# Kernel tuning notes

Hardware: AMD Instinct MI355X
Metric: run time of the kernel (lower is better)

Reference implementation:

```python
import jax, jax.numpy as jnp
import numpy as np

N_NODES = 50000
N_EDGES = 800000
DROP_P = 0.1


def setup_inputs() -> dict:
    key = jax.random.key(0)
    ks = jax.random.split(key, 8)
    x = jax.random.normal(ks[0], (N_NODES, 128), dtype=jnp.float32)
    edge_index = jax.random.randint(ks[1], (2, N_EDGES), 0, N_NODES, dtype=jnp.int64)
    # SAGEConv params: lin_l (applied to aggregated neighbors, has bias), lin_r (root, no bias)
    Wl1 = jax.random.normal(ks[2], (128, 256), dtype=jnp.float32) * 0.05
    Wr1 = jax.random.normal(ks[3], (128, 256), dtype=jnp.float32) * 0.05
    b1 = jax.random.normal(ks[4], (256,), dtype=jnp.float32) * 0.05
    Wl2 = jax.random.normal(ks[5], (256, 128), dtype=jnp.float32) * 0.05
    Wr2 = jax.random.normal(ks[6], (256, 128), dtype=jnp.float32) * 0.05
    b2 = jax.random.normal(ks[7], (128,), dtype=jnp.float32) * 0.05
    return {"x": x, "edge_index": edge_index, "Wl1": Wl1, "Wr1": Wr1, "b1": b1,
            "Wl2": Wl2, "Wr2": Wr2, "b2": b2}


def _sage_conv(x, src, dst, Wl, Wr, b, n_nodes):
    # PyG SAGEConv (mean aggr): out = lin_l(mean_{j in N(i)} x_j) + lin_r(x_i)
    msg = x[src]                                                  # [E, d] gather
    agg = jax.ops.segment_sum(msg, dst, num_segments=n_nodes)    # [N, d]
    cnt = jax.ops.segment_sum(jnp.ones((src.shape[0],), x.dtype), dst, num_segments=n_nodes)
    mean = agg / jnp.maximum(cnt, 1.0)[:, None]
    return mean @ Wl + x @ Wr + b


def reference(x, edge_index, Wl1, Wr1, b1, Wl2, Wr2, b2):
    src, dst = edge_index[0], edge_index[1]
    n = x.shape[0]
    h = _sage_conv(x, src, dst, Wl1, Wr1, b1, n)
    h = jax.nn.relu(h)
    # dropout p=0.1 with deterministic key (training=True in source)
    keep = jax.random.bernoulli(jax.random.key(42), 1.0 - DROP_P, h.shape)
    h = jnp.where(keep, h / (1.0 - DROP_P), 0.0)
    return _sage_conv(h, src, dst, Wl2, Wr2, b2, n)
```

## Files before the change

kernel.cpp:

```cpp
#include <hip/hip_runtime.h>

#define NN 50000
#define NE 800000
#define NBC 49
#define MSB 391

typedef __attribute__((ext_vector_type(8))) short short8;
typedef __attribute__((ext_vector_type(4))) float f32x4;

#define GLDS(g, l)                                                              \
  __builtin_amdgcn_global_load_lds(                                             \
      (const __attribute__((address_space(1))) void*)(g),                       \
      (__attribute__((address_space(3))) void*)(l), 16, 0, 0)

__device__ __forceinline__ unsigned short f2bf(float f) {
  union { float f; unsigned u; } v; v.f = f;
  unsigned r = (v.u + 0x7FFFu + ((v.u >> 16) & 1u)) >> 16;
  return (unsigned short)r;
}
__device__ __forceinline__ float bflo(unsigned u) {
  union { unsigned x; float f; } v; v.x = u << 16; return v.f;
}
__device__ __forceinline__ float bfhi(unsigned u) {
  union { unsigned x; float f; } v; v.x = u & 0xFFFF0000u; return v.f;
}

__device__ __forceinline__ unsigned tf_rotl(unsigned x, int r) {
#if __has_builtin(__builtin_amdgcn_alignbit)
  return __builtin_amdgcn_alignbit(x, x, 32 - r);
#else
  return (x << r) | (x >> (32 - r));
#endif
}
__device__ __forceinline__ void threefry_0_42(unsigned x0, unsigned x1,
                                              unsigned& o0, unsigned& o1) {
  const unsigned k0 = 0u, k1 = 42u;
  const unsigned k2 = k0 ^ k1 ^ 0x1BD11BDAu;
  x0 += k0; x1 += k1;
#define TF_R(r) { x0 += x1; x1 = tf_rotl(x1, (r)); x1 ^= x0; }
  TF_R(13) TF_R(15) TF_R(26) TF_R(6)
  x0 += k1; x1 += k2 + 1u;
  TF_R(17) TF_R(29) TF_R(16) TF_R(24)
  x0 += k2; x1 += k0 + 2u;
  TF_R(13) TF_R(15) TF_R(26) TF_R(6)
  x0 += k0; x1 += k1 + 3u;
  TF_R(17) TF_R(29) TF_R(16) TF_R(24)
  x0 += k1; x1 += k2 + 4u;
  TF_R(13) TF_R(15) TF_R(26) TF_R(6)
  x0 += k2; x1 += k0 + 5u;
#undef TF_R
  o0 = x0; o1 = x1;
}
__device__ __forceinline__ float dropout_scale(unsigned flat) {
  unsigned o0, o1;
  threefry_0_42(0u, flat, o0, o1);
  unsigned bits = o0 ^ o1;
  return ((bits >> 9) < 7549747u) ? (1.0f / 0.9f) : 0.0f;
}

#define CVTB 6250
__global__ void prep_k(const float4* __restrict__ x, uint2* __restrict__ xb,
                       const float* __restrict__ Wl1, const float* __restrict__ Wr1,
                       const float* __restrict__ Wl2, const float* __restrict__ Wr2,
                       unsigned short* __restrict__ W1t, unsigned short* __restrict__ W2t,
                       unsigned* __restrict__ hist) {
  int bid = blockIdx.x;
  if (bid < CVTB) {
    int i = bid * 256 + threadIdx.x;
    float4 v = x[i];
    uint2 o;
    o.x = (unsigned)f2bf(v.x) | ((unsigned)f2bf(v.y) << 16);
    o.y = (unsigned)f2bf(v.z) | ((unsigned)f2bf(v.w) << 16);
    xb[i] = o;
  } else if (bid < CVTB + 512) {
    int gid = (bid - CVTB) * 256 + threadIdx.x;
    int idx = gid & 65535;
    int n = idx >> 8, k = idx & 255;
    if (gid < 65536) {
      float v = (k < 128) ? Wr1[(size_t)k * 256 + n] : Wl1[(size_t)(k - 128) * 256 + n];
      W1t[idx] = f2bf(v);
    } else {
      float v = (n < 128) ? Wl2[(size_t)k * 128 + n] : Wr2[(size_t)k * 128 + (n - 128)];
      W2t[idx] = f2bf(v);
    }
  } else {
    if (threadIdx.x < 64) hist[threadIdx.x] = 0;
  }
}

__global__ __launch_bounds__(256) void histC_k(const int* __restrict__ dst,
                                               unsigned* __restrict__ hist) {
  __shared__ unsigned lh[64];
  int tid = threadIdx.x;
  if (tid < 64) lh[tid] = 0;
  __syncthreads();
  int base = blockIdx.x * 2048;
#pragma unroll
  for (int k = 0; k < 8; ++k) {
    int e = base + k * 256 + tid;
    if (e < NE) atomicAdd(&lh[((unsigned)dst[e]) >> 10], 1u);
  }
  __syncthreads();
  if (tid < 64 && lh[tid]) atomicAdd(&hist[tid], lh[tid]);
}

__global__ __launch_bounds__(64) void scan64_k(const unsigned* __restrict__ hist,
                                               unsigned* __restrict__ bases,
                                               unsigned* __restrict__ gcur) {
  int tid = threadIdx.x;
  unsigned v = hist[tid], incl = v;
#pragma unroll
  for (int o = 1; o < 64; o <<= 1) {
    unsigned t = __shfl_up(incl, o);
    if (tid >= o) incl += t;
  }
  unsigned ex = incl - v;
  bases[tid] = ex;
  gcur[tid] = ex;
  if (tid == 63) bases[64] = incl;
}

__global__ __launch_bounds__(256) void msplit_k(const int* __restrict__ src,
                                                const int* __restrict__ dst,
                                                unsigned* __restrict__ gcur,
                                                unsigned* __restrict__ bufA) {
  __shared__ unsigned lh[64], gb[64], lc[64];
  int tid = threadIdx.x;
  if (tid < 64) { lh[tid] = 0; lc[tid] = 0; }
  __syncthreads();
  int base = blockIdx.x * 2048;
  unsigned s[8], d[8];
  bool val[8];
#pragma unroll
  for (int k = 0; k < 8; ++k) {
    int e = base + k * 256 + tid;
    val[k] = (e < NE);
    s[k] = val[k] ? (unsigned)src[e] : 0u;
    d[k] = val[k] ? (unsigned)dst[e] : 0u;
    if (val[k]) atomicAdd(&lh[d[k] >> 10], 1u);
  }
  __syncthreads();
  if (tid < 64 && lh[tid]) gb[tid] = atomicAdd(&gcur[tid], lh[tid]);
  __syncthreads();
#pragma unroll
  for (int k = 0; k < 8; ++k) {
    if (val[k]) {
      unsigned b = d[k] >> 10;
      unsigned pos = atomicAdd(&lc[b], 1u);
      bufA[gb[b] + pos] = (s[k] & 0xFFFFu) | ((d[k] & 1023u) << 16);
    }
  }
}

__global__ __launch_bounds__(1024) void passB2_k(const unsigned* __restrict__ bases,
                                                 const unsigned* __restrict__ bufA,
                                                 unsigned short* __restrict__ esrc,
                                                 unsigned* __restrict__ rowptr,
                                                 float* __restrict__ inv) {
  __shared__ unsigned cnt[1024], offs[1024], s_[1024];
  __shared__ unsigned short stage[18432];
  const int b = blockIdx.x, tid = threadIdx.x;
  const unsigned base0 = bases[b];
  const unsigned end0 = bases[b + 1];
  const unsigned bcnt = end0 - base0;

  cnt[tid] = 0;
  __syncthreads();
  for (unsigned i = tid; i < bcnt; i += 1024)
    atomicAdd(&cnt[bufA[base0 + i] >> 16], 1u);
  __syncthreads();

  unsigned c = cnt[tid];
  s_[tid] = c;
  __syncthreads();
  for (int o = 1; o < 1024; o <<= 1) {
    unsigned t = (tid >= o) ? s_[tid - o] : 0u;
    __syncthreads();
    s_[tid] += t;
    __syncthreads();
  }
  unsigned ex = s_[tid] - c;
  offs[tid] = ex;
  int node = b * 1024 + tid;
  if (node < NN) {
    rowptr[node] = base0 + ex;
    inv[node] = 1.0f / fmaxf((float)c, 1.0f);
  }
  cnt[tid] = 0;
  if (b == NBC - 1 && tid == 0) rowptr[NN] = NE;
  __syncthreads();

  if (bcnt <= 18432) {
    for (unsigned i = tid; i < bcnt; i += 1024) {
      unsigned w = bufA[base0 + i];
      unsigned dl = w >> 16;
      unsigned pos = atomicAdd(&cnt[dl], 1u);
      stage[offs[dl] + pos] = (unsigned short)w;
    }
    __syncthreads();
    for (unsigned i = tid; i < bcnt; i += 1024) esrc[base0 + i] = stage[i];
  } else {
    for (unsigned i = tid; i < bcnt; i += 1024) {
      unsigned w = bufA[base0 + i];
      unsigned dl = w >> 16;
      unsigned pos = atomicAdd(&cnt[dl], 1u);
      esrc[base0 + offs[dl] + pos] = (unsigned short)w;
    }
  }
}

__global__ __launch_bounds__(256) void gather_mean_k(
    const unsigned short* __restrict__ esrc, const unsigned* __restrict__ rowptr,
    const float* __restrict__ inv, const unsigned* __restrict__ xb,
    unsigned* __restrict__ meanb) {
  int node = blockIdx.x * 4 + (threadIdx.x >> 6);
  if (node >= NN) return;
  int lane = threadIdx.x & 63;
  unsigned beg = rowptr[node], end = rowptr[node + 1];
  float ax = 0.f, ay = 0.f;
  unsigned t = beg;
  for (; t + 8 <= end; t += 8) {
    unsigned v0 = xb[(size_t)esrc[t + 0] * 64 + lane];
    unsigned v1 = xb[(size_t)esrc[t + 1] * 64 + lane];
    unsigned v2 = xb[(size_t)esrc[t + 2] * 64 + lane];
    unsigned v3 = xb[(size_t)esrc[t + 3] * 64 + lane];
    unsigned v4 = xb[(size_t)esrc[t + 4] * 64 + lane];
    unsigned v5 = xb[(size_t)esrc[t + 5] * 64 + lane];
    unsigned v6 = xb[(size_t)esrc[t + 6] * 64 + lane];
    unsigned v7 = xb[(size_t)esrc[t + 7] * 64 + lane];
    ax += ((bflo(v0) + bflo(v1)) + (bflo(v2) + bflo(v3))) +
          ((bflo(v4) + bflo(v5)) + (bflo(v6) + bflo(v7)));
    ay += ((bfhi(v0) + bfhi(v1)) + (bfhi(v2) + bfhi(v3))) +
          ((bfhi(v4) + bfhi(v5)) + (bfhi(v6) + bfhi(v7)));
  }
  for (; t + 4 <= end; t += 4) {
    unsigned v0 = xb[(size_t)esrc[t + 0] * 64 + lane];
    unsigned v1 = xb[(size_t)esrc[t + 1] * 64 + lane];
    unsigned v2 = xb[(size_t)esrc[t + 2] * 64 + lane];
    unsigned v3 = xb[(size_t)esrc[t + 3] * 64 + lane];
    ax += (bflo(v0) + bflo(v1)) + (bflo(v2) + bflo(v3));
    ay += (bfhi(v0) + bfhi(v1)) + (bfhi(v2) + bfhi(v3));
  }
  for (; t < end; ++t) {
    unsigned v0 = xb[(size_t)esrc[t] * 64 + lane];
    ax += bflo(v0); ay += bfhi(v0);
  }
  float sc = inv[node];
  meanb[(size_t)node * 64 + lane] =
      (unsigned)f2bf(ax * sc) | ((unsigned)f2bf(ay * sc) << 16);
}

__global__ __launch_bounds__(256) void gather_add_k(
    const unsigned short* __restrict__ esrc, const unsigned* __restrict__ rowptr,
    const float* __restrict__ inv, const unsigned* __restrict__ P,
    float* __restrict__ out) {
  int node = blockIdx.x * 4 + (threadIdx.x >> 6);
  if (node >= NN) return;
  int lane = threadIdx.x & 63;
  unsigned beg = rowptr[node], end = rowptr[node + 1];
  float ax = 0.f, ay = 0.f;
  unsigned t = beg;
  for (; t + 8 <= end; t += 8) {
    unsigned v0 = P[(size_t)esrc[t + 0] * 64 + lane];
    unsigned v1 = P[(size_t)esrc[t + 1] * 64 + lane];
    unsigned v2 = P[(size_t)esrc[t + 2] * 64 + lane];
    unsigned v3 = P[(size_t)esrc[t + 3] * 64 + lane];
    unsigned v4 = P[(size_t)esrc[t + 4] * 64 + lane];
    unsigned v5 = P[(size_t)esrc[t + 5] * 64 + lane];
    unsigned v6 = P[(size_t)esrc[t + 6] * 64 + lane];
    unsigned v7 = P[(size_t)esrc[t + 7] * 64 + lane];
    ax += ((bflo(v0) + bflo(v1)) + (bflo(v2) + bflo(v3))) +
          ((bflo(v4) + bflo(v5)) + (bflo(v6) + bflo(v7)));
    ay += ((bfhi(v0) + bfhi(v1)) + (bfhi(v2) + bfhi(v3))) +
          ((bfhi(v4) + bfhi(v5)) + (bfhi(v6) + bfhi(v7)));
  }
  for (; t + 4 <= end; t += 4) {
    unsigned v0 = P[(size_t)esrc[t + 0] * 64 + lane];
    unsigned v1 = P[(size_t)esrc[t + 1] * 64 + lane];
    unsigned v2 = P[(size_t)esrc[t + 2] * 64 + lane];
    unsigned v3 = P[(size_t)esrc[t + 3] * 64 + lane];
    ax += (bflo(v0) + bflo(v1)) + (bflo(v2) + bflo(v3));
    ay += (bfhi(v0) + bfhi(v1)) + (bfhi(v2) + bfhi(v3));
  }
  for (; t < end; ++t) {
    unsigned v0 = P[(size_t)esrc[t] * 64 + lane];
    ax += bflo(v0); ay += bfhi(v0);
  }
  float sc = inv[node];
  float2* O = (float2*)out;
  float2 o = O[(size_t)node * 64 + lane];
  o.x += ax * sc;
  o.y += ay * sc;
  O[(size_t)node * 64 + lane] = o;
}


__global__ __launch_bounds__(256) void mgemm1_k(
    const unsigned short* __restrict__ xb, const unsigned short* __restrict__ meanb,
    const unsigned short* __restrict__ W1t, const float* __restrict__ b1,
    unsigned short* __restrict__ h) {
  __shared__ __align__(16) char As[64 * 64 * 2];
  __shared__ __align__(16) char Bs[64 * 64 * 2];
  const int tid = threadIdx.x;
  const int lane = tid & 63, wid = tid >> 6;
  const int wm = (wid >> 1) * 32, wn = (wid & 1) * 32;
  const int r16 = lane & 15, g = lane >> 4;
  const unsigned bid = blockIdx.x;
  const unsigned v_ = (bid & 7u) * 391u + (bid >> 3);
  const int m0 = (int)(v_ >> 2) * 64;
  const int j0 = (int)(v_ & 3u) * 64;
  const int wbase = (tid & ~63);

  const unsigned short* aSrcX[2];
  const unsigned short* aSrcM[2];
  const unsigned short* bSrc[2];
  char* ldsA[2];
  char* ldsB[2];
#pragma unroll
  for (int p = 0; p < 2; ++p) {
    int id = p * 256 + tid;
    int r = id >> 3, cb = id & 7;
    int grow = m0 + r;
    if (grow >= NN) grow = NN - 1;
    int swz = (cb ^ (r & 7)) << 3;
    aSrcX[p] = xb + (size_t)grow * 128 + swz;
    aSrcM[p] = meanb + (size_t)grow * 128 + swz;
    bSrc[p] = W1t + (size_t)(j0 + r) * 256 + swz;
    ldsA[p] = As + ((p * 256 + wbase) << 4);
    ldsB[p] = Bs + ((p * 256 + wbase) << 4);
  }

  int aoff[2][2], boff[2][2];
#pragma unroll
  for (int f = 0; f < 2; ++f)
#pragma unroll
    for (int ks = 0; ks < 2; ++ks) {
      int ar = wm + f * 16 + r16;
      aoff[f][ks] = ar * 128 + ((ks * 64 + g * 16) ^ ((ar & 7) << 4));
      int br = wn + f * 16 + r16;
      boff[f][ks] = br * 128 + ((ks * 64 + g * 16) ^ ((br & 7) << 4));
    }

  f32x4 acc[2][2] = {};

  auto compute = [&]() {
#pragma unroll
    for (int ks = 0; ks < 2; ++ks) {
      short8 af[2], bf[2];
#pragma unroll
      for (int f = 0; f < 2; ++f) {
        af[f] = *(const short8*)(As + aoff[f][ks]);
        bf[f] = *(const short8*)(Bs + boff[f][ks]);
      }
#pragma unroll
      for (int i = 0; i < 2; ++i)
#pragma unroll
        for (int j = 0; j < 2; ++j)
          acc[i][j] = __builtin_amdgcn_mfma_f32_16x16x32_bf16(af[i], bf[j], acc[i][j], 0, 0, 0);
    }
  };

  GLDS(aSrcX[0], ldsA[0]); GLDS(aSrcX[1], ldsA[1]);
  GLDS(bSrc[0], ldsB[0]);  GLDS(bSrc[1], ldsB[1]);

  float dsc[2][2][4];
#pragma unroll
  for (int i = 0; i < 2; ++i)
#pragma unroll
    for (int j = 0; j < 2; ++j) {
      int col = j0 + wn + j * 16 + r16;
#pragma unroll
      for (int q = 0; q < 4; ++q) {
        int row = m0 + wm + i * 16 + g * 4 + q;
        dsc[i][j][q] = dropout_scale((unsigned)row * 256u + (unsigned)col);
      }
    }

  __syncthreads();
  compute();
  __syncthreads();
  GLDS(aSrcX[0] + 64, ldsA[0]); GLDS(aSrcX[1] + 64, ldsA[1]);
  GLDS(bSrc[0] + 64, ldsB[0]);  GLDS(bSrc[1] + 64, ldsB[1]);
  __syncthreads();
  compute();
  __syncthreads();
  GLDS(aSrcM[0], ldsA[0]);       GLDS(aSrcM[1], ldsA[1]);
  GLDS(bSrc[0] + 128, ldsB[0]);  GLDS(bSrc[1] + 128, ldsB[1]);
  __syncthreads();
  compute();
  __syncthreads();
  GLDS(aSrcM[0] + 64, ldsA[0]);  GLDS(aSrcM[1] + 64, ldsA[1]);
  GLDS(bSrc[0] + 192, ldsB[0]);  GLDS(bSrc[1] + 192, ldsB[1]);
  __syncthreads();
  compute();

#pragma unroll
  for (int i = 0; i < 2; ++i)
#pragma unroll
    for (int j = 0; j < 2; ++j) {
      int col = j0 + wn + j * 16 + r16;
      float bias = b1[col];
#pragma unroll
      for (int q = 0; q < 4; ++q) {
        int row = m0 + wm + i * 16 + g * 4 + q;
        if (row < NN) {
          float v = fmaxf(acc[i][j][q] + bias, 0.f) * dsc[i][j][q];
          h[(size_t)row * 256 + col] = f2bf(v);
        }
      }
    }
}

__global__ __launch_bounds__(256) void mgemm2_k(
    const unsigned short* __restrict__ h, const unsigned short* __restrict__ W2t,
    const float* __restrict__ b2, unsigned short* __restrict__ P,
    float* __restrict__ out) {
  __shared__ __align__(16) char As[64 * 64 * 2];
  __shared__ __align__(16) char Bs[64 * 64 * 2];
  const int tid = threadIdx.x;
  const int lane = tid & 63, wid = tid >> 6;
  const int wm = (wid >> 1) * 32, wn = (wid & 1) * 32;
  const int r16 = lane & 15, g = lane >> 4;
  const unsigned bid = blockIdx.x;
  const unsigned v_ = (bid & 7u) * 391u + (bid >> 3);
  const int m0 = (int)(v_ >> 2) * 64;
  const int j0 = (int)(v_ & 3u) * 64;
  const int wbase = (tid & ~63);

  const unsigned short* aSrc[2];
  const unsigned short* bSrc[2];
  char* ldsA[2];
  char* ldsB[2];
#pragma unroll
  for (int p = 0; p < 2; ++p) {
    int id = p * 256 + tid;
    int r = id >> 3, cb = id & 7;
    int grow = m0 + r;
    if (grow >= NN) grow = NN - 1;
    int swz = (cb ^ (r & 7)) << 3;
    aSrc[p] = h + (size_t)grow * 256 + swz;
    bSrc[p] = W2t + (size_t)(j0 + r) * 256 + swz;
    ldsA[p] = As + ((p * 256 + wbase) << 4);
    ldsB[p] = Bs + ((p * 256 + wbase) << 4);
  }

  int aoff[2][2], boff[2][2];
#pragma unroll
  for (int f = 0; f < 2; ++f)
#pragma unroll
    for (int ks = 0; ks < 2; ++ks) {
      int ar = wm + f * 16 + r16;
      aoff[f][ks] = ar * 128 + ((ks * 64 + g * 16) ^ ((ar & 7) << 4));
      int br = wn + f * 16 + r16;
      boff[f][ks] = br * 128 + ((ks * 64 + g * 16) ^ ((br & 7) << 4));
    }

  f32x4 acc[2][2] = {};

  auto compute = [&]() {
#pragma unroll
    for (int ks = 0; ks < 2; ++ks) {
      short8 af[2], bf[2];
#pragma unroll
      for (int f = 0; f < 2; ++f) {
        af[f] = *(const short8*)(As + aoff[f][ks]);
        bf[f] = *(const short8*)(Bs + boff[f][ks]);
      }
#pragma unroll
      for (int i = 0; i < 2; ++i)
#pragma unroll
        for (int j = 0; j < 2; ++j)
          acc[i][j] = __builtin_amdgcn_mfma_f32_16x16x32_bf16(af[i], bf[j], acc[i][j], 0, 0, 0);
    }
  };

  GLDS(aSrc[0], ldsA[0]); GLDS(aSrc[1], ldsA[1]);
  GLDS(bSrc[0], ldsB[0]); GLDS(bSrc[1], ldsB[1]);
  __syncthreads();
  compute();
  __syncthreads();
  GLDS(aSrc[0] + 64, ldsA[0]); GLDS(aSrc[1] + 64, ldsA[1]);
  GLDS(bSrc[0] + 64, ldsB[0]); GLDS(bSrc[1] + 64, ldsB[1]);
  __syncthreads();
  compute();
  __syncthreads();
  GLDS(aSrc[0] + 128, ldsA[0]); GLDS(aSrc[1] + 128, ldsA[1]);
  GLDS(bSrc[0] + 128, ldsB[0]); GLDS(bSrc[1] + 128, ldsB[1]);
  __syncthreads();
  compute();
  __syncthreads();
  GLDS(aSrc[0] + 192, ldsA[0]); GLDS(aSrc[1] + 192, ldsA[1]);
  GLDS(bSrc[0] + 192, ldsB[0]); GLDS(bSrc[1] + 192, ldsB[1]);
  __syncthreads();
  compute();

#pragma unroll
  for (int i = 0; i < 2; ++i)
#pragma unroll
    for (int j = 0; j < 2; ++j) {
      int col = j0 + wn + j * 16 + r16;
#pragma unroll
      for (int q = 0; q < 4; ++q) {
        int row = m0 + wm + i * 16 + g * 4 + q;
        if (row < NN) {
          if (col < 128) {
            P[(size_t)row * 128 + col] = f2bf(acc[i][j][q]);
          } else {
            out[(size_t)row * 128 + (col - 128)] = acc[i][j][q] + b2[col - 128];
          }
        }
      }
    }
}

extern "C" void kernel_launch(void* const* d_in, const int* in_sizes, int n_in,
                              void* d_out, int out_size, void* d_ws, size_t ws_size,
                              hipStream_t stream) {
  const float* x   = (const float*)d_in[0];
  const int*   ei  = (const int*)d_in[1];
  const float* Wl1 = (const float*)d_in[2];
  const float* Wr1 = (const float*)d_in[3];
  const float* b1  = (const float*)d_in[4];
  const float* Wl2 = (const float*)d_in[5];
  const float* Wr2 = (const float*)d_in[6];
  const float* b2  = (const float*)d_in[7];
  float* out = (float*)d_out;

  const int* src = ei;
  const int* dst = ei + NE;

  char* ws = (char*)d_ws;
  unsigned*       rowptr = (unsigned*)ws;
  float*          inv    = (float*)(ws + 0x40000);
  unsigned*       hist   = (unsigned*)(ws + 0x80000);
  unsigned*       bases  = (unsigned*)(ws + 0x80400);
  unsigned*       gcur   = (unsigned*)(ws + 0x80800);
  unsigned short* esrc   = (unsigned short*)(ws + 0xC0000);
  unsigned*       bufA   = (unsigned*)(ws + 0x280000);
  unsigned short* W1t    = (unsigned short*)(ws + 0x600000);
  unsigned short* W2t    = (unsigned short*)(ws + 0x620000);
  unsigned short* xb     = (unsigned short*)(ws + 0x700000);
  unsigned short* meanb  = (unsigned short*)(ws + 0x1400000);
  unsigned short* h      = (unsigned short*)(ws + 0x2100000);
  unsigned short* P      = (unsigned short*)(ws + 0x3A00000);

  const int TPB = 256;

  prep_k<<<CVTB + 513, TPB, 0, stream>>>((const float4*)x, (uint2*)xb,
                                         Wl1, Wr1, Wl2, Wr2, W1t, W2t, hist);

  histC_k<<<MSB, TPB, 0, stream>>>(dst, hist);
  scan64_k<<<1, 64, 0, stream>>>(hist, bases, gcur);
  msplit_k<<<MSB, TPB, 0, stream>>>(src, dst, gcur, bufA);
  passB2_k<<<NBC, 1024, 0, stream>>>(bases, bufA, esrc, rowptr, inv);

  gather_mean_k<<<(NN + 3) / 4, TPB, 0, stream>>>(esrc, rowptr, inv, (const unsigned*)xb, (unsigned*)meanb);
  mgemm1_k<<<3128, TPB, 0, stream>>>(xb, meanb, W1t, b1, h);

  mgemm2_k<<<3128, TPB, 0, stream>>>(h, W2t, b2, P, out);
  gather_add_k<<<(NN + 3) / 4, TPB, 0, stream>>>(esrc, rowptr, inv, (const unsigned*)P, out);
}
```

Baseline: 171.1 us.

## Split CSR scatter blocks in half and vectorize edge index loads in gathers

```diff
diff --git a/kernel.cpp b/kernel.cpp
--- a/kernel.cpp
+++ b/kernel.cpp
@@ -159,9 +159,11 @@
                                                  float* __restrict__ inv) {
   __shared__ unsigned cnt[1024], offs[1024], s_[1024];
   __shared__ unsigned short stage[18432];
-  const int b = blockIdx.x, tid = threadIdx.x;
-  const unsigned base0 = bases[b];
-  const unsigned end0 = bases[b + 1];
+  const int bk = blockIdx.x >> 1;
+  const int half = blockIdx.x & 1;
+  const int tid = threadIdx.x;
+  const unsigned base0 = bases[bk];
+  const unsigned end0 = bases[bk + 1];
   const unsigned bcnt = end0 - base0;
 
   cnt[tid] = 0;
@@ -181,30 +183,40 @@
   }
   unsigned ex = s_[tid] - c;
   offs[tid] = ex;
-  int node = b * 1024 + tid;
-  if (node < NN) {
-    rowptr[node] = base0 + ex;
-    inv[node] = 1.0f / fmaxf((float)c, 1.0f);
+  const int lo = half * 512;
+  if (tid >= lo && tid < lo + 512) {
+    int node = bk * 1024 + tid;
+    if (node < NN) {
+      rowptr[node] = base0 + ex;
+      inv[node] = 1.0f / fmaxf((float)c, 1.0f);
+    }
   }
   cnt[tid] = 0;
-  if (b == NBC - 1 && tid == 0) rowptr[NN] = NE;
-  __syncthreads();
-
-  if (bcnt <= 18432) {
+  if (bk == NBC - 1 && half == 0 && tid == 0) rowptr[NN] = NE;
+  __syncthreads();
+
+  const unsigned hbase = offs[lo];
+  const unsigned hcnt = half ? (bcnt - offs[512]) : offs[512];
+
+  if (hcnt <= 18432) {
     for (unsigned i = tid; i < bcnt; i += 1024) {
       unsigned w = bufA[base0 + i];
       unsigned dl = w >> 16;
-      unsigned pos = atomicAdd(&cnt[dl], 1u);
-      stage[offs[dl] + pos] = (unsigned short)w;
+      if ((int)(dl >> 9) == half) {
+        unsigned pos = atomicAdd(&cnt[dl], 1u);
+        stage[offs[dl] - hbase + pos] = (unsigned short)w;
+      }
     }
     __syncthreads();
-    for (unsigned i = tid; i < bcnt; i += 1024) esrc[base0 + i] = stage[i];
+    for (unsigned i = tid; i < hcnt; i += 1024) esrc[base0 + hbase + i] = stage[i];
   } else {
     for (unsigned i = tid; i < bcnt; i += 1024) {
       unsigned w = bufA[base0 + i];
       unsigned dl = w >> 16;
-      unsigned pos = atomicAdd(&cnt[dl], 1u);
-      esrc[base0 + offs[dl] + pos] = (unsigned short)w;
+      if ((int)(dl >> 9) == half) {
+        unsigned pos = atomicAdd(&cnt[dl], 1u);
+        esrc[base0 + offs[dl] + pos] = (unsigned short)w;
+      }
     }
   }
 }
@@ -219,27 +231,34 @@
   unsigned beg = rowptr[node], end = rowptr[node + 1];
   float ax = 0.f, ay = 0.f;
   unsigned t = beg;
+  for (; t < end && (t & 7u); ++t) {
+    unsigned v0 = xb[(size_t)esrc[t] * 64 + lane];
+    ax += bflo(v0); ay += bfhi(v0);
+  }
   for (; t + 8 <= end; t += 8) {
-    unsigned v0 = xb[(size_t)esrc[t + 0] * 64 + lane];
-    unsigned v1 = xb[(size_t)esrc[t + 1] * 64 + lane];
-    unsigned v2 = xb[(size_t)esrc[t + 2] * 64 + lane];
-    unsigned v3 = xb[(size_t)esrc[t + 3] * 64 + lane];
-    unsigned v4 = xb[(size_t)esrc[t + 4] * 64 + lane];
-    unsigned v5 = xb[(size_t)esrc[t + 5] * 64 + lane];
-    unsigned v6 = xb[(size_t)esrc[t + 6] * 64 + lane];
-    unsigned v7 = xb[(size_t)esrc[t + 7] * 64 + lane];
+    uint4 iw = *(const uint4*)(esrc + t);
+    unsigned v0 = xb[(size_t)(iw.x & 0xFFFFu) * 64 + lane];
+    unsigned v1 = xb[(size_t)(iw.x >> 16) * 64 + lane];
+    unsigned v2 = xb[(size_t)(iw.y & 0xFFFFu) * 64 + lane];
+    unsigned v3 = xb[(size_t)(iw.y >> 16) * 64 + lane];
+    unsigned v4 = xb[(size_t)(iw.z & 0xFFFFu) * 64 + lane];
+    unsigned v5 = xb[(size_t)(iw.z >> 16) * 64 + lane];
+    unsigned v6 = xb[(size_t)(iw.w & 0xFFFFu) * 64 + lane];
+    unsigned v7 = xb[(size_t)(iw.w >> 16) * 64 + lane];
     ax += ((bflo(v0) + bflo(v1)) + (bflo(v2) + bflo(v3))) +
           ((bflo(v4) + bflo(v5)) + (bflo(v6) + bflo(v7)));
     ay += ((bfhi(v0) + bfhi(v1)) + (bfhi(v2) + bfhi(v3))) +
           ((bfhi(v4) + bfhi(v5)) + (bfhi(v6) + bfhi(v7)));
   }
-  for (; t + 4 <= end; t += 4) {
-    unsigned v0 = xb[(size_t)esrc[t + 0] * 64 + lane];
-    unsigned v1 = xb[(size_t)esrc[t + 1] * 64 + lane];
-    unsigned v2 = xb[(size_t)esrc[t + 2] * 64 + lane];
-    unsigned v3 = xb[(size_t)esrc[t + 3] * 64 + lane];
+  if (t + 4 <= end) {
+    uint2 iw = *(const uint2*)(esrc + t);
+    unsigned v0 = xb[(size_t)(iw.x & 0xFFFFu) * 64 + lane];
+    unsigned v1 = xb[(size_t)(iw.x >> 16) * 64 + lane];
+    unsigned v2 = xb[(size_t)(iw.y & 0xFFFFu) * 64 + lane];
+    unsigned v3 = xb[(size_t)(iw.y >> 16) * 64 + lane];
     ax += (bflo(v0) + bflo(v1)) + (bflo(v2) + bflo(v3));
     ay += (bfhi(v0) + bfhi(v1)) + (bfhi(v2) + bfhi(v3));
+    t += 4;
   }
   for (; t < end; ++t) {
     unsigned v0 = xb[(size_t)esrc[t] * 64 + lane];
@@ -260,27 +279,34 @@
   unsigned beg = rowptr[node], end = rowptr[node + 1];
   float ax = 0.f, ay = 0.f;
   unsigned t = beg;
+  for (; t < end && (t & 7u); ++t) {
+    unsigned v0 = P[(size_t)esrc[t] * 64 + lane];
+    ax += bflo(v0); ay += bfhi(v0);
+  }
   for (; t + 8 <= end; t += 8) {
-    unsigned v0 = P[(size_t)esrc[t + 0] * 64 + lane];
-    unsigned v1 = P[(size_t)esrc[t + 1] * 64 + lane];
-    unsigned v2 = P[(size_t)esrc[t + 2] * 64 + lane];
-    unsigned v3 = P[(size_t)esrc[t + 3] * 64 + lane];
-    unsigned v4 = P[(size_t)esrc[t + 4] * 64 + lane];
-    unsigned v5 = P[(size_t)esrc[t + 5] * 64 + lane];
-    unsigned v6 = P[(size_t)esrc[t + 6] * 64 + lane];
-    unsigned v7 = P[(size_t)esrc[t + 7] * 64 + lane];
+    uint4 iw = *(const uint4*)(esrc + t);
+    unsigned v0 = P[(size_t)(iw.x & 0xFFFFu) * 64 + lane];
+    unsigned v1 = P[(size_t)(iw.x >> 16) * 64 + lane];
+    unsigned v2 = P[(size_t)(iw.y & 0xFFFFu) * 64 + lane];
+    unsigned v3 = P[(size_t)(iw.y >> 16) * 64 + lane];
+    unsigned v4 = P[(size_t)(iw.z & 0xFFFFu) * 64 + lane];
+    unsigned v5 = P[(size_t)(iw.z >> 16) * 64 + lane];
+    unsigned v6 = P[(size_t)(iw.w & 0xFFFFu) * 64 + lane];
+    unsigned v7 = P[(size_t)(iw.w >> 16) * 64 + lane];
     ax += ((bflo(v0) + bflo(v1)) + (bflo(v2) + bflo(v3))) +
           ((bflo(v4) + bflo(v5)) + (bflo(v6) + bflo(v7)));
     ay += ((bfhi(v0) + bfhi(v1)) + (bfhi(v2) + bfhi(v3))) +
           ((bfhi(v4) + bfhi(v5)) + (bfhi(v6) + bfhi(v7)));
   }
-  for (; t + 4 <= end; t += 4) {
-    unsigned v0 = P[(size_t)esrc[t + 0] * 64 + lane];
-    unsigned v1 = P[(size_t)esrc[t + 1] * 64 + lane];
-    unsigned v2 = P[(size_t)esrc[t + 2] * 64 + lane];
-    unsigned v3 = P[(size_t)esrc[t + 3] * 64 + lane];
+  if (t + 4 <= end) {
+    uint2 iw = *(const uint2*)(esrc + t);
+    unsigned v0 = P[(size_t)(iw.x & 0xFFFFu) * 64 + lane];
+    unsigned v1 = P[(size_t)(iw.x >> 16) * 64 + lane];
+    unsigned v2 = P[(size_t)(iw.y & 0xFFFFu) * 64 + lane];
+    unsigned v3 = P[(size_t)(iw.y >> 16) * 64 + lane];
     ax += (bflo(v0) + bflo(v1)) + (bflo(v2) + bflo(v3));
     ay += (bfhi(v0) + bfhi(v1)) + (bfhi(v2) + bfhi(v3));
+    t += 4;
   }
   for (; t < end; ++t) {
     unsigned v0 = P[(size_t)esrc[t] * 64 + lane];
@@ -293,7 +319,6 @@
   o.y += ay * sc;
   O[(size_t)node * 64 + lane] = o;
 }
-
 
 __global__ __launch_bounds__(256) void mgemm1_k(
     const unsigned short* __restrict__ xb, const unsigned short* __restrict__ meanb,
@@ -552,7 +577,7 @@
   histC_k<<<MSB, TPB, 0, stream>>>(dst, hist);
   scan64_k<<<1, 64, 0, stream>>>(hist, bases, gcur);
   msplit_k<<<MSB, TPB, 0, stream>>>(src, dst, gcur, bufA);
-  passB2_k<<<NBC, 1024, 0, stream>>>(bases, bufA, esrc, rowptr, inv);
+  passB2_k<<<NBC * 2, 1024, 0, stream>>>(bases, bufA, esrc, rowptr, inv);
 
   gather_mean_k<<<(NN + 3) / 4, TPB, 0, stream>>>(esrc, rowptr, inv, (const unsigned*)xb, (unsigned*)meanb);
   mgemm1_k<<<3128, TPB, 0, stream>>>(xb, meanb, W1t, b1, h);
```

After: 191.7 us. 12.0% more time.
